# Kernel tuning notes

Hardware: AMD Instinct MI355X
Metric: run time of the kernel (lower is better)

Reference implementation:

```python
import jax, jax.numpy as jnp
import numpy as np

BLOCK = 16
NUM_HEADS = 12
EMBED = 768
LN_EPS = 1e-6


def setup_inputs() -> dict:
    key = jax.random.key(0)
    ks = jax.random.split(key, 6)
    H = W = 1024
    x = jax.random.normal(ks[0], (H, W), dtype=jnp.float32)
    # Conv2d(1, EMBED, kernel=BLOCK, stride=BLOCK) weights, flattened to [E, b*b]
    proj_w = jax.random.normal(ks[1], (EMBED, BLOCK * BLOCK), dtype=jnp.float32) * 0.02
    proj_b = jax.random.normal(ks[2], (EMBED,), dtype=jnp.float32) * 0.02
    ln_g = jnp.ones((EMBED,), dtype=jnp.float32)
    ln_b = jnp.zeros((EMBED,), dtype=jnp.float32)
    # nn.Linear(E, 3E, bias=False): weight [3E, E]
    qkv_w = jax.random.normal(ks[3], (3 * EMBED, EMBED), dtype=jnp.float32) * 0.02
    return {"x": x, "proj_w": proj_w, "proj_b": proj_b,
            "ln_g": ln_g, "ln_b": ln_b, "qkv_w": qkv_w}


def reference(x, proj_w, proj_b, ln_g, ln_b, qkv_w):
    H, W = x.shape
    b = BLOCK
    # Patch embed: conv with kernel=stride=b on a single-channel image is
    # exactly patchify + matmul. Token order matches flatten(2) (row-major).
    patches = x.reshape(H // b, b, W // b, b).transpose(0, 2, 1, 3)
    patches = patches.reshape((H // b) * (W // b), b * b)      # [N, b*b]
    tok = patches @ proj_w.T + proj_b                          # [N, E]

    # LayerNorm (eps=1e-6)
    mu = jnp.mean(tok, axis=-1, keepdims=True)
    var = jnp.mean(jnp.square(tok - mu), axis=-1, keepdims=True)
    tok = (tok - mu) * jax.lax.rsqrt(var + LN_EPS) * ln_g + ln_b

    # Attention (batch = 1)
    N, C = tok.shape
    h, d = NUM_HEADS, C // NUM_HEADS
    qkv = (tok @ qkv_w.T).reshape(N, 3, h, d)                  # [N, 3, h, d]
    q = qkv[:, 0].transpose(1, 0, 2)                            # [h, N, d]
    k = qkv[:, 1].transpose(1, 0, 2)
    v = qkv[:, 2].transpose(1, 0, 2)
    scale = d ** -0.5
    attn = jax.nn.softmax(jnp.einsum('hnd,hmd->hnm', q, k) * scale, axis=-1)
    out = jnp.einsum('hnm,hmd->hnd', attn, v)                   # [h, N, d]
    out = out.transpose(1, 0, 2).reshape(N, C)                  # [N, C]
    return out[None]                                            # [1, N, C]
```

## Files before the change

kernel.cpp:

```cpp
#include <hip/hip_runtime.h>
#include <hip/hip_bf16.h>

typedef __bf16 bf16_t;
typedef __attribute__((ext_vector_type(8))) __bf16 bf16x8;
typedef __attribute__((ext_vector_type(4))) __bf16 bf16x4;
typedef __attribute__((ext_vector_type(4))) float f32x4;
typedef __attribute__((ext_vector_type(4))) unsigned int uint4v;

#define QSCALE 0.1803368801111204f

static __device__ inline void glds16(const bf16_t* g, bf16_t* l) {
    __builtin_amdgcn_global_load_lds(
        (__attribute__((address_space(1))) const void*)g,
        (__attribute__((address_space(3))) void*)l,
        16, 0, 0);
}

static __device__ inline float hwexp2(float x) {
#if __has_builtin(__builtin_amdgcn_exp2f)
    return __builtin_amdgcn_exp2f(x);
#else
    float r;
    asm("v_exp_f32 %0, %1" : "=v"(r) : "v"(x));
    return r;
#endif
}

static __device__ inline unsigned int pack_trunc(float lo, float hi) {
    return __builtin_amdgcn_perm(__builtin_bit_cast(unsigned int, hi),
                                 __builtin_bit_cast(unsigned int, lo),
                                 0x07060302u);
}

__global__ void cvt_kernel(const float* __restrict__ in, bf16_t* __restrict__ out, int n4) {
    int i = blockIdx.x * 256 + threadIdx.x;
    if (i < n4) {
        float4 v = ((const float4*)in)[i];
        bf16x4 o = {(bf16_t)v.x, (bf16_t)v.y, (bf16_t)v.z, (bf16_t)v.w};
        ((bf16x4*)out)[i] = o;
    }
}

__global__ __launch_bounds__(256) void patch_gemm(const float* __restrict__ x,
                                                  const float* __restrict__ pw,
                                                  const float* __restrict__ pb,
                                                  float* __restrict__ tok) {
    const int bn = blockIdx.x;
    const int bm = blockIdx.y;
    const int tid = threadIdx.x;

    __shared__ bf16_t At[64][264];
    __shared__ bf16_t Bt[64][264];

    #pragma unroll
    for (int t = 0; t < 16; t++) {
        int linear = tid + t * 256;
        int ml = linear >> 6;
        int kv = (linear & 63) << 2;
        int n = bm * 64 + ml;
        int pr = n >> 6, pc = n & 63;
        int i = kv >> 4, j = kv & 15;
        float4 v = *(const float4*)(x + (pr * 16 + i) * 1024 + pc * 16 + j);
        bf16x4 o = {(bf16_t)v.x, (bf16_t)v.y, (bf16_t)v.z, (bf16_t)v.w};
        *(bf16x4*)(&At[ml][kv]) = o;
    }
    #pragma unroll
    for (int t = 0; t < 8; t++) {
        int linear = tid + t * 256;
        int nl = linear >> 5;
        int kv = (linear & 31) << 3;
        const float* src = pw + (size_t)(bn * 64 + nl) * 256 + kv;
        float4 v0 = *(const float4*)(src);
        float4 v1 = *(const float4*)(src + 4);
        bf16x8 o = {(bf16_t)v0.x, (bf16_t)v0.y, (bf16_t)v0.z, (bf16_t)v0.w,
                    (bf16_t)v1.x, (bf16_t)v1.y, (bf16_t)v1.z, (bf16_t)v1.w};
        *(bf16x8*)(&Bt[nl][kv]) = o;
    }
    __syncthreads();

    const int lane = tid & 63, wid = tid >> 6, ln = lane & 15, quad = lane >> 4;
    f32x4 acc[4];
    #pragma unroll
    for (int s = 0; s < 4; s++) acc[s] = {0.f, 0.f, 0.f, 0.f};

    #pragma unroll
    for (int kk = 0; kk < 8; kk++) {
        bf16x8 af = *(const bf16x8*)(&At[wid * 16 + ln][kk * 32 + quad * 8]);
        #pragma unroll
        for (int s = 0; s < 4; s++) {
            bf16x8 bfr = *(const bf16x8*)(&Bt[s * 16 + ln][kk * 32 + quad * 8]);
            acc[s] = __builtin_amdgcn_mfma_f32_16x16x32_bf16(af, bfr, acc[s], 0, 0, 0);
        }
    }

    #pragma unroll
    for (int s = 0; s < 4; s++) {
        int e = bn * 64 + s * 16 + ln;
        float bias = pb[e];
        #pragma unroll
        for (int r = 0; r < 4; r++) {
            int m = bm * 64 + wid * 16 + quad * 4 + r;
            tok[(size_t)m * 768 + e] = acc[s][r] + bias;
        }
    }
}

__global__ __launch_bounds__(256) void ln_kernel(const float* __restrict__ tok,
                                                 const float* __restrict__ g,
                                                 const float* __restrict__ b,
                                                 bf16_t* __restrict__ out) {
    const int n = blockIdx.x;
    const int tid = threadIdx.x;
    const float* row = tok + (size_t)n * 768;
    float x0 = row[tid], x1 = row[tid + 256], x2 = row[tid + 512];
    float s = x0 + x1 + x2;
    float s2 = x0 * x0 + x1 * x1 + x2 * x2;
    #pragma unroll
    for (int off = 32; off; off >>= 1) {
        s += __shfl_xor(s, off);
        s2 += __shfl_xor(s2, off);
    }
    __shared__ float ws1[4], ws2[4];
    int wid = tid >> 6;
    if ((tid & 63) == 0) { ws1[wid] = s; ws2[wid] = s2; }
    __syncthreads();
    s = ws1[0] + ws1[1] + ws1[2] + ws1[3];
    s2 = ws2[0] + ws2[1] + ws2[2] + ws2[3];
    float mu = s * (1.f / 768.f);
    float var = s2 * (1.f / 768.f) - mu * mu;
    float r = rsqrtf(var + 1e-6f);
    bf16_t* orow = out + (size_t)n * 768;
    orow[tid]       = (bf16_t)((x0 - mu) * r * g[tid]       + b[tid]);
    orow[tid + 256] = (bf16_t)((x1 - mu) * r * g[tid + 256] + b[tid + 256]);
    orow[tid + 512] = (bf16_t)((x2 - mu) * r * g[tid + 512] + b[tid + 512]);
}

__global__ __launch_bounds__(256) void qkv_gemm(const bf16_t* __restrict__ tokb,
                                                const bf16_t* __restrict__ wq,
                                                bf16_t* __restrict__ qb,
                                                bf16_t* __restrict__ kswz,
                                                bf16_t* __restrict__ vswz) {
    const int bn = blockIdx.x;
    const int bm = blockIdx.y;
    const int tid = threadIdx.x;
    const int wid = tid >> 6, lane = tid & 63;
    const int ln = lane & 15, quad = lane >> 4;
    const int wm = wid & 1, wn = wid >> 1;

    __shared__ bf16_t Asw[2][8192];
    __shared__ bf16_t Bsw[2][4096];

    f32x4 acc[4][2];
    #pragma unroll
    for (int sm = 0; sm < 4; sm++)
        #pragma unroll
        for (int sn = 0; sn < 2; sn++) acc[sm][sn] = {0.f, 0.f, 0.f, 0.f};

    auto stage = [&](int kb0, int buf) {
        #pragma unroll
        for (int i = 0; i < 4; i++) {
            int L = wid * 256 + i * 64 + lane;
            int r = L >> 3, c = L & 7;
            int gc = c ^ (r & 7);
            glds16(tokb + (size_t)(bm * 128 + r) * 768 + kb0 + gc * 8,
                   Asw[buf] + (wid * 256 + i * 64) * 8);
        }
        #pragma unroll
        for (int i = 0; i < 2; i++) {
            int L = wid * 128 + i * 64 + lane;
            int r = L >> 3, c = L & 7;
            int gc = c ^ (r & 7);
            glds16(wq + (size_t)(bn * 64 + r) * 768 + kb0 + gc * 8,
                   Bsw[buf] + (wid * 128 + i * 64) * 8);
        }
    };

    auto compute = [&](const bf16_t* Ab, const bf16_t* Bb) {
        #pragma unroll
        for (int kk = 0; kk < 2; kk++) {
            const int c = (kk * 4 + quad) ^ (ln & 7);
            bf16x8 af[4], bfr[2];
            #pragma unroll
            for (int sm = 0; sm < 4; sm++) {
                int row = wm * 64 + sm * 16 + ln;
                af[sm] = *(const bf16x8*)(Ab + (row * 8 + c) * 8);
            }
            #pragma unroll
            for (int sn = 0; sn < 2; sn++) {
                int row = wn * 32 + sn * 16 + ln;
                bfr[sn] = *(const bf16x8*)(Bb + (row * 8 + c) * 8);
            }
            #pragma unroll
            for (int sm = 0; sm < 4; sm++)
                #pragma unroll
                for (int sn = 0; sn < 2; sn++)
                    acc[sm][sn] = __builtin_amdgcn_mfma_f32_16x16x32_bf16(af[sm], bfr[sn], acc[sm][sn], 0, 0, 0);
        }
    };

    stage(0, 0);

    for (int s = 0; s < 12; s += 2) {
        __builtin_amdgcn_s_barrier();
        stage((s + 1) * 64, 1);
        __builtin_amdgcn_s_waitcnt(0x0F76);
        __builtin_amdgcn_s_barrier();
        compute(Asw[0], Bsw[0]);
        __builtin_amdgcn_s_barrier();
        if (s + 2 < 12) {
            stage((s + 2) * 64, 0);
            __builtin_amdgcn_s_waitcnt(0x0F76);
        } else {
            __builtin_amdgcn_s_waitcnt(0x0F70);
        }
        __builtin_amdgcn_s_barrier();
        compute(Asw[1], Bsw[1]);
    }

    const int sidx = bn / 12;
    const int head = bn % 12;
    #pragma unroll
    for (int sn = 0; sn < 2; sn++) {
        int dc = wn * 32 + sn * 16 + ln;
        #pragma unroll
        for (int sm = 0; sm < 4; sm++) {
            #pragma unroll
            for (int r = 0; r < 4; r++) {
                int m = bm * 128 + wm * 64 + sm * 16 + quad * 4 + r;
                float v = acc[sm][sn][r];
                if (sidx == 0) {
                    qb[((size_t)(head * 4096 + m)) * 64 + dc] = (bf16_t)(v * QSCALE);
                } else if (sidx == 1) {
                    bf16_t val = (bf16_t)v;
                    int kt = m >> 6, sb = (m >> 4) & 3, lnk = m & 15;
                    int half = dc >> 5, quadk = (dc >> 3) & 3, j = dc & 7;
                    int l = quadk * 16 + lnk;
                    kswz[((size_t)(head * 64 + kt)) * 4096 + sb * 1024 + half * 512 + l * 8 + j] = val;
                } else {
                    bf16_t val = (bf16_t)v;
                    int kt = m >> 6, keyl = m & 63;
                    int sblk = keyl >> 4;
                    int mm = sblk >> 1, tb = sblk & 1;
                    int w16 = keyl & 15, qv = w16 >> 2, jj = w16 & 3;
                    int jp = tb * 4 + jj;
                    int db = dc >> 4, lnv = dc & 15;
                    int l = qv * 16 + lnv;
                    vswz[((size_t)(head * 64 + kt)) * 4096 + ((mm * 4 + db) * 64 + l) * 8 + jp] = val;
                }
            }
        }
    }
}

__global__ __launch_bounds__(256, 4) void attn_partial(const bf16_t* __restrict__ qbuf,
                                                       const bf16_t* __restrict__ kswz,
                                                       const bf16_t* __restrict__ vswz,
                                                       float* __restrict__ raw0,
                                                       float* __restrict__ raw1,
                                                       float* __restrict__ l_part) {
    const int h = blockIdx.y;
    const int chunk = blockIdx.z;
    const int tid = threadIdx.x;
    const int wid = tid >> 6;
    const int lane = tid & 63;
    const int ln = lane & 15, quad = lane >> 4;
    const int qh = wid & 1;
    const int kh = wid >> 1;
    const int q0 = blockIdx.x * 64;

    __shared__ __align__(16) char RAW[32768];
    bf16_t* Kst = (bf16_t*)RAW;
    bf16_t* Vst = (bf16_t*)(RAW + 16384);

    bf16x8 qf[2][2];
    #pragma unroll
    for (int g = 0; g < 2; g++) {
        const int q0g = q0 + qh * 32 + g * 16;
        const bf16_t* qrow = qbuf + ((size_t)h * 4096 + q0g + ln) * 64;
        qf[g][0] = *(const bf16x8*)(qrow + quad * 8);
        qf[g][1] = *(const bf16x8*)(qrow + 32 + quad * 8);
    }

    bf16x8 ones;
    #pragma unroll
    for (int i = 0; i < 8; i++) ones[i] = (bf16_t)1.0f;

    const bf16_t* kg = kswz + (size_t)h * 64 * 4096 + (size_t)(chunk * 32 + kh * 16) * 4096;
    const bf16_t* vg = vswz + (size_t)h * 64 * 4096 + (size_t)(chunk * 32 + kh * 16) * 4096;

    f32x4 accO[2][4];
    f32x4 accL[2];
    #pragma unroll
    for (int g = 0; g < 2; g++) {
        accL[g] = {0.f, 0.f, 0.f, 0.f};
        #pragma unroll
        for (int d = 0; d < 4; d++) accO[g][d] = {0.f, 0.f, 0.f, 0.f};
    }

    auto stage = [&](int ht, int buf) {
        const bf16_t* kt_g = kg + (size_t)ht * 2048;
        const bf16_t* vt_g = vg + (size_t)ht * 2048;
        bf16_t* kl = Kst + (kh * 2 + buf) * 2048 + qh * 1024;
        bf16_t* vl = Vst + (kh * 2 + buf) * 2048 + qh * 1024;
        #pragma unroll
        for (int i = 0; i < 2; i++) {
            glds16(kt_g + qh * 1024 + i * 512 + lane * 8, kl + i * 512);
            glds16(vt_g + qh * 1024 + i * 512 + lane * 8, vl + i * 512);
        }
    };

    auto compute = [&](const bf16_t* Kb, const bf16_t* Vb) {
        bf16x8 vf0 = *(const bf16x8*)(Vb + 0 * 512 + lane * 8);
        bf16x8 vf1 = *(const bf16x8*)(Vb + 1 * 512 + lane * 8);
        bf16x8 vf2 = *(const bf16x8*)(Vb + 2 * 512 + lane * 8);
        bf16x8 vf3 = *(const bf16x8*)(Vb + 3 * 512 + lane * 8);
        bf16x8 ka0 = *(const bf16x8*)(Kb + lane * 8);
        bf16x8 ka1 = *(const bf16x8*)(Kb + 512 + lane * 8);
        bf16x8 kb0 = *(const bf16x8*)(Kb + 1024 + lane * 8);
        bf16x8 kb1 = *(const bf16x8*)(Kb + 1536 + lane * 8);
        #pragma unroll
        for (int g = 0; g < 2; g++) {
            f32x4 z = {0.f, 0.f, 0.f, 0.f};
            f32x4 SA = __builtin_amdgcn_mfma_f32_16x16x32_bf16(ka0, qf[g][0], z, 0, 0, 0);
            SA = __builtin_amdgcn_mfma_f32_16x16x32_bf16(ka1, qf[g][1], SA, 0, 0, 0);
            unsigned int u0 = pack_trunc(hwexp2(SA[0]), hwexp2(SA[1]));
            unsigned int u1 = pack_trunc(hwexp2(SA[2]), hwexp2(SA[3]));
            f32x4 SB = __builtin_amdgcn_mfma_f32_16x16x32_bf16(kb0, qf[g][0], z, 0, 0, 0);
            SB = __builtin_amdgcn_mfma_f32_16x16x32_bf16(kb1, qf[g][1], SB, 0, 0, 0);
            unsigned int u2 = pack_trunc(hwexp2(SB[0]), hwexp2(SB[1]));
            unsigned int u3 = pack_trunc(hwexp2(SB[2]), hwexp2(SB[3]));
            uint4v u = {u0, u1, u2, u3};
            bf16x8 pb = __builtin_bit_cast(bf16x8, u);
            accL[g] = __builtin_amdgcn_mfma_f32_16x16x32_bf16(ones, pb, accL[g], 0, 0, 0);
            accO[g][0] = __builtin_amdgcn_mfma_f32_16x16x32_bf16(vf0, pb, accO[g][0], 0, 0, 0);
            accO[g][1] = __builtin_amdgcn_mfma_f32_16x16x32_bf16(vf1, pb, accO[g][1], 0, 0, 0);
            accO[g][2] = __builtin_amdgcn_mfma_f32_16x16x32_bf16(vf2, pb, accO[g][2], 0, 0, 0);
            accO[g][3] = __builtin_amdgcn_mfma_f32_16x16x32_bf16(vf3, pb, accO[g][3], 0, 0, 0);
        }
    };

    stage(0, 0);

    const bf16_t* K0 = Kst + (kh * 2 + 0) * 2048;
    const bf16_t* V0 = Vst + (kh * 2 + 0) * 2048;
    const bf16_t* K1 = Kst + (kh * 2 + 1) * 2048;
    const bf16_t* V1 = Vst + (kh * 2 + 1) * 2048;

    for (int ht = 0; ht < 32; ht += 2) {
        __builtin_amdgcn_s_barrier();
        stage(ht + 1, 1);
        __builtin_amdgcn_s_waitcnt(0x0F74);
        __builtin_amdgcn_s_barrier();
        compute(K0, V0);
        __builtin_amdgcn_s_barrier();
        if (ht + 2 < 32) {
            stage(ht + 2, 0);
            __builtin_amdgcn_s_waitcnt(0x0F74);
        } else {
            __builtin_amdgcn_s_waitcnt(0x0F70);
        }
        __builtin_amdgcn_s_barrier();
        compute(K1, V1);
    }

    __syncthreads();
    float* comb  = (float*)RAW;
    float* combl = (float*)(RAW + 17408);
    if (kh == 1) {
        #pragma unroll
        for (int g = 0; g < 2; g++) {
            const int lq = qh * 32 + g * 16 + ln;
            #pragma unroll
            for (int db = 0; db < 4; db++)
                *(f32x4*)&comb[lq * 68 + db * 16 + quad * 4] = accO[g][db];
            if (quad == 0) combl[lq] = accL[g][0];
        }
    }
    __syncthreads();
    if (kh == 0) {
        float* base = chunk ? raw1 : raw0;
        #pragma unroll
        for (int g = 0; g < 2; g++) {
            const int lq = qh * 32 + g * 16 + ln;
            const int qg = q0 + lq;
            float lsum = accL[g][0] + combl[lq];
            if (quad == 0) l_part[(size_t)chunk * 49152 + h * 4096 + qg] = lsum;
            float* op = base + (size_t)qg * 768 + h * 64 + quad * 4;
            #pragma unroll
            for (int db = 0; db < 4; db++) {
                f32x4 o = accO[g][db] + *(const f32x4*)&comb[lq * 68 + db * 16 + quad * 4];
                *(f32x4*)(op + db * 16) = o;
            }
        }
    }
}

__global__ __launch_bounds__(256) void norm_kernel(const float* __restrict__ raw0,
                                                   const float* __restrict__ raw1,
                                                   const float* __restrict__ l_part,
                                                   float* __restrict__ out) {
    const int q = blockIdx.x;
    const int tid = threadIdx.x;
    __shared__ float linv[12];
    if (tid < 12)
        linv[tid] = 1.0f / (l_part[tid * 4096 + q] + l_part[49152 + tid * 4096 + q]);
    __syncthreads();
    #pragma unroll
    for (int t = 0; t < 3; t++) {
        int c = tid + t * 256;
        size_t idx = (size_t)q * 768 + c;
        out[idx] = (raw0[idx] + raw1[idx]) * linv[c >> 6];
    }
}

extern "C" void kernel_launch(void* const* d_in, const int* in_sizes, int n_in,
                              void* d_out, int out_size, void* d_ws, size_t ws_size,
                              hipStream_t stream) {
    const float* x      = (const float*)d_in[0];
    const float* proj_w = (const float*)d_in[1];
    const float* proj_b = (const float*)d_in[2];
    const float* ln_g   = (const float*)d_in[3];
    const float* ln_b   = (const float*)d_in[4];
    const float* qkv_w  = (const float*)d_in[5];
    float* out = (float*)d_out;

    char* ws = (char*)d_ws;
    float*  tok_pre = (float*)(ws + 0);
    bf16_t* tok_b   = (bf16_t*)(ws + 12582912);
    bf16_t* pw_b    = (bf16_t*)(ws + 18874368);
    bf16_t* qw_b    = (bf16_t*)(ws + 19267584);
    bf16_t* qbuf    = (bf16_t*)(ws + 22806528);
    bf16_t* kswz    = (bf16_t*)(ws + 29097984);
    bf16_t* vswz    = (bf16_t*)(ws + 35389440);
    float*  raw0    = tok_pre;
    float*  raw1    = out;
    float*  l_part  = (float*)pw_b;

    cvt_kernel<<<1728, 256, 0, stream>>>(qkv_w, qw_b, 442368);
    patch_gemm<<<dim3(12, 64), 256, 0, stream>>>(x, proj_w, proj_b, tok_pre);
    ln_kernel<<<4096, 256, 0, stream>>>(tok_pre, ln_g, ln_b, tok_b);
    qkv_gemm<<<dim3(36, 32), 256, 0, stream>>>(tok_b, qw_b, qbuf, kswz, vswz);
    attn_partial<<<dim3(64, 12, 2), 256, 0, stream>>>(qbuf, kswz, vswz, raw0, raw1, l_part);
    norm_kernel<<<4096, 256, 0, stream>>>(raw0, raw1, l_part, out);
}
```

Baseline: 176.9 us.

## Drop split-K attention and norm kernel; merge weight conversion into patch GEMM

Each attention block now covers all 64 key tiles itself instead of splitting keys across two chunks. The softmax normalization is applied in the epilogue, which removes the separate norm kernel and the fp32 partial-output round trip through memory. The qkv weight fp32-to-bf16 conversion is folded into the patch GEMM launch as extra blocks, saving one launch. The attention grid halves to 768 blocks, so fewer blocks are in flight to hide latency on the GPU, and each block runs twice as long.

```diff
diff --git a/kernel.cpp b/kernel.cpp
--- a/kernel.cpp
+++ b/kernel.cpp
@@ -32,22 +32,25 @@
                                  0x07060302u);
 }
 
-__global__ void cvt_kernel(const float* __restrict__ in, bf16_t* __restrict__ out, int n4) {
-    int i = blockIdx.x * 256 + threadIdx.x;
-    if (i < n4) {
-        float4 v = ((const float4*)in)[i];
+__global__ __launch_bounds__(256) void prep_kernel(const float* __restrict__ x,
+                                                   const float* __restrict__ pw,
+                                                   const float* __restrict__ pb,
+                                                   float* __restrict__ tok,
+                                                   const float* __restrict__ qkv_w,
+                                                   bf16_t* __restrict__ qw_b) {
+    const int tid = threadIdx.x;
+
+    if (blockIdx.y >= 64) {
+        int id = (blockIdx.y - 64) * 12 + blockIdx.x;
+        int i = id * 256 + tid;
+        float4 v = ((const float4*)qkv_w)[i];
         bf16x4 o = {(bf16_t)v.x, (bf16_t)v.y, (bf16_t)v.z, (bf16_t)v.w};
-        ((bf16x4*)out)[i] = o;
-    }
-}
-
-__global__ __launch_bounds__(256) void patch_gemm(const float* __restrict__ x,
-                                                  const float* __restrict__ pw,
-                                                  const float* __restrict__ pb,
-                                                  float* __restrict__ tok) {
+        ((bf16x4*)qw_b)[i] = o;
+        return;
+    }
+
     const int bn = blockIdx.x;
     const int bm = blockIdx.y;
-    const int tid = threadIdx.x;
 
     __shared__ bf16_t At[64][264];
     __shared__ bf16_t Bt[64][264];
@@ -252,14 +255,11 @@
     }
 }
 
-__global__ __launch_bounds__(256, 4) void attn_partial(const bf16_t* __restrict__ qbuf,
-                                                       const bf16_t* __restrict__ kswz,
-                                                       const bf16_t* __restrict__ vswz,
-                                                       float* __restrict__ raw0,
-                                                       float* __restrict__ raw1,
-                                                       float* __restrict__ l_part) {
+__global__ __launch_bounds__(256, 4) void attn_full(const bf16_t* __restrict__ qbuf,
+                                                    const bf16_t* __restrict__ kswz,
+                                                    const bf16_t* __restrict__ vswz,
+                                                    float* __restrict__ out) {
     const int h = blockIdx.y;
-    const int chunk = blockIdx.z;
     const int tid = threadIdx.x;
     const int wid = tid >> 6;
     const int lane = tid & 63;
@@ -285,8 +285,8 @@
     #pragma unroll
     for (int i = 0; i < 8; i++) ones[i] = (bf16_t)1.0f;
 
-    const bf16_t* kg = kswz + (size_t)h * 64 * 4096 + (size_t)(chunk * 32 + kh * 16) * 4096;
-    const bf16_t* vg = vswz + (size_t)h * 64 * 4096 + (size_t)(chunk * 32 + kh * 16) * 4096;
+    const bf16_t* kg = kswz + (size_t)h * 64 * 4096 + (size_t)(kh * 32) * 4096;
+    const bf16_t* vg = vswz + (size_t)h * 64 * 4096 + (size_t)(kh * 32) * 4096;
 
     f32x4 accO[2][4];
     f32x4 accL[2];
@@ -346,14 +346,14 @@
     const bf16_t* K1 = Kst + (kh * 2 + 1) * 2048;
     const bf16_t* V1 = Vst + (kh * 2 + 1) * 2048;
 
-    for (int ht = 0; ht < 32; ht += 2) {
+    for (int ht = 0; ht < 64; ht += 2) {
         __builtin_amdgcn_s_barrier();
         stage(ht + 1, 1);
         __builtin_amdgcn_s_waitcnt(0x0F74);
         __builtin_amdgcn_s_barrier();
         compute(K0, V0);
         __builtin_amdgcn_s_barrier();
-        if (ht + 2 < 32) {
+        if (ht + 2 < 64) {
             stage(ht + 2, 0);
             __builtin_amdgcn_s_waitcnt(0x0F74);
         } else {
@@ -378,38 +378,19 @@
     }
     __syncthreads();
     if (kh == 0) {
-        float* base = chunk ? raw1 : raw0;
         #pragma unroll
         for (int g = 0; g < 2; g++) {
             const int lq = qh * 32 + g * 16 + ln;
             const int qg = q0 + lq;
-            float lsum = accL[g][0] + combl[lq];
-            if (quad == 0) l_part[(size_t)chunk * 49152 + h * 4096 + qg] = lsum;
-            float* op = base + (size_t)qg * 768 + h * 64 + quad * 4;
+            float inv = 1.0f / (accL[g][0] + combl[lq]);
+            float* op = out + (size_t)qg * 768 + h * 64 + quad * 4;
             #pragma unroll
             for (int db = 0; db < 4; db++) {
-                f32x4 o = accO[g][db] + *(const f32x4*)&comb[lq * 68 + db * 16 + quad * 4];
+                f32x4 o = (accO[g][db] + *(const f32x4*)&comb[lq * 68 + db * 16 + quad * 4]);
+                o *= inv;
                 *(f32x4*)(op + db * 16) = o;
             }
         }
-    }
-}
-
-__global__ __launch_bounds__(256) void norm_kernel(const float* __restrict__ raw0,
-                                                   const float* __restrict__ raw1,
-                                                   const float* __restrict__ l_part,
-                                                   float* __restrict__ out) {
-    const int q = blockIdx.x;
-    const int tid = threadIdx.x;
-    __shared__ float linv[12];
-    if (tid < 12)
-        linv[tid] = 1.0f / (l_part[tid * 4096 + q] + l_part[49152 + tid * 4096 + q]);
-    __syncthreads();
-    #pragma unroll
-    for (int t = 0; t < 3; t++) {
-        int c = tid + t * 256;
-        size_t idx = (size_t)q * 768 + c;
-        out[idx] = (raw0[idx] + raw1[idx]) * linv[c >> 6];
     }
 }
 
@@ -427,19 +408,13 @@
     char* ws = (char*)d_ws;
     float*  tok_pre = (float*)(ws + 0);
     bf16_t* tok_b   = (bf16_t*)(ws + 12582912);
-    bf16_t* pw_b    = (bf16_t*)(ws + 18874368);
-    bf16_t* qw_b    = (bf16_t*)(ws + 19267584);
-    bf16_t* qbuf    = (bf16_t*)(ws + 22806528);
-    bf16_t* kswz    = (bf16_t*)(ws + 29097984);
-    bf16_t* vswz    = (bf16_t*)(ws + 35389440);
-    float*  raw0    = tok_pre;
-    float*  raw1    = out;
-    float*  l_part  = (float*)pw_b;
-
-    cvt_kernel<<<1728, 256, 0, stream>>>(qkv_w, qw_b, 442368);
-    patch_gemm<<<dim3(12, 64), 256, 0, stream>>>(x, proj_w, proj_b, tok_pre);
+    bf16_t* qw_b    = (bf16_t*)(ws + 18874368);
+    bf16_t* qbuf    = (bf16_t*)(ws + 22413312);
+    bf16_t* kswz    = (bf16_t*)(ws + 28704768);
+    bf16_t* vswz    = (bf16_t*)(ws + 34996224);
+
+    prep_kernel<<<dim3(12, 208), 256, 0, stream>>>(x, proj_w, proj_b, tok_pre, qkv_w, qw_b);
     ln_kernel<<<4096, 256, 0, stream>>>(tok_pre, ln_g, ln_b, tok_b);
     qkv_gemm<<<dim3(36, 32), 256, 0, stream>>>(tok_b, qw_b, qbuf, kswz, vswz);
-    attn_partial<<<dim3(64, 12, 2), 256, 0, stream>>>(qbuf, kswz, vswz, raw0, raw1, l_part);
-    norm_kernel<<<4096, 256, 0, stream>>>(raw0, raw1, l_part, out);
-}
+    attn_full<<<dim3(64, 12), 256, 0, stream>>>(qbuf, kswz, vswz, out);
+}
```

Measured after the change: 171.3 us. -3.2%, faster.
